# Kernel tuning notes

Measured on AMD Instinct MI355X. Metric: run time of the kernel, lower is better.

The kernel has to match this reference:

```python
import jax, jax.numpy as jnp
import numpy as np

N_HEADS = 16
D_EMBED = 1024


def setup_inputs() -> dict:
    key = jax.random.key(0)
    k_x, k_win, k_bin, k_wout, k_bout = jax.random.split(key, 5)
    B, S, D = 4, 2048, D_EMBED
    # weights stored as (in, out) so y = x @ W + b (equivalent to torch Linear)
    x = jax.random.normal(k_x, (B, S, D), dtype=jnp.float32)
    W_in = jax.random.normal(k_win, (D, 3 * D), dtype=jnp.float32) * (D ** -0.5)
    b_in = jax.random.normal(k_bin, (3 * D,), dtype=jnp.float32) * 0.02
    W_out = jax.random.normal(k_wout, (D, D), dtype=jnp.float32) * (D ** -0.5)
    b_out = jax.random.normal(k_bout, (D,), dtype=jnp.float32) * 0.02
    return {"x": x, "W_in": W_in, "b_in": b_in, "W_out": W_out, "b_out": b_out,
            "causal_mask": 1}


def reference(x, W_in, b_in, W_out, b_out, causal_mask):
    B, S, D = x.shape
    H = N_HEADS
    dh = D // H
    qkv = x @ W_in + b_in                      # [B,S,3D]
    q, k, v = jnp.split(qkv, 3, axis=-1)
    q = q.reshape(B, S, H, dh)
    k = k.reshape(B, S, H, dh)
    v = v.reshape(B, S, H, dh)
    scores = jnp.einsum('bqhd,bkhd->bhqk', q, k)   # [B,H,S,S]
    if causal_mask:
        # original masks with -inf BEFORE scaling; -inf/sqrt(dh) == -inf
        tri = jnp.triu(jnp.ones((S, S), dtype=bool), k=1)
        scores = jnp.where(tri, -jnp.inf, scores)
    scores = scores / jnp.sqrt(jnp.asarray(dh, dtype=scores.dtype))
    attn = jax.nn.softmax(scores, axis=-1)
    out = jnp.einsum('bhqk,bkhd->bqhd', attn, v).reshape(B, S, D)
    return out @ W_out + b_out
```

## Files before the change

kernel.cpp:

```cpp
#include <hip/hip_runtime.h>
#include <hip/hip_bf16.h>
#include <stdint.h>
#include <string.h>

#define S_LEN 2048
#define NH    16
#define DH    64
#define D_EMB 1024
#define CSCALE 0.18033688011112042f

typedef __attribute__((ext_vector_type(8)))  short short8;
typedef __attribute__((ext_vector_type(4)))  float f32x4;
typedef __attribute__((ext_vector_type(16))) float f32x16;
typedef __attribute__((ext_vector_type(4)))  uint32_t u32x4;

__device__ __forceinline__ unsigned short f2bf(float f) {
  uint32_t u = __builtin_bit_cast(uint32_t, f);
  uint32_t r = (u + 0x7FFFu + ((u >> 16) & 1u)) >> 16;
  return (unsigned short)r;
}

__device__ __forceinline__ uint32_t pkbf(float a, float b) {
  float2 f; f.x = a; f.y = b;
  __hip_bfloat162 h = __float22bfloat162_rn(f);
  uint32_t r;
  memcpy(&r, &h, 4);
  return r;
}

__device__ __forceinline__ uint32_t pktr(float a, float b) {
  return __builtin_amdgcn_perm(__builtin_bit_cast(uint32_t, b),
                               __builtin_bit_cast(uint32_t, a), 0x07060302u);
}

__device__ __forceinline__ float fexp2(float x) {
#if __has_builtin(__builtin_amdgcn_exp2f)
  return __builtin_amdgcn_exp2f(x);
#else
  float r;
  asm("v_exp_f32 %0, %1\ns_nop 0" : "=v"(r) : "v"(x));
  return r;
#endif
}

__device__ __forceinline__ void gload16(const void* g, void* l) {
  __builtin_amdgcn_global_load_lds(
      (__attribute__((address_space(1))) void*)(g),
      (__attribute__((address_space(3))) void*)(l),
      16, 0, 0);
}

__device__ __forceinline__ f32x16 mfma32(short8 a, short8 b, f32x16 c) {
  return __builtin_amdgcn_mfma_f32_32x32x16_bf16(a, b, c, 0, 0, 0);
}


__global__ __launch_bounds__(256)
void cvt_bf16(const float* __restrict__ in, unsigned short* __restrict__ out, int n) {
  int i = (blockIdx.x * 256 + threadIdx.x) * 4;
  if (i >= n) return;
  float4 v = *(const float4*)&in[i];
  ushort4 o;
  o.x = f2bf(v.x); o.y = f2bf(v.y); o.z = f2bf(v.z); o.w = f2bf(v.w);
  *(ushort4*)&out[i] = o;
}

__global__ __launch_bounds__(256)
void transpose_cvt(const float* __restrict__ in, unsigned short* __restrict__ out,
                   int R, int C) {
  __shared__ float t[64][65];
  const int nbr = R >> 6;
  const int br = (blockIdx.x % nbr) << 6;
  const int bc = (blockIdx.x / nbr) << 6;
  const int tid = threadIdx.x;
  const int tr = tid >> 4;
  const int tc = (tid & 15) << 2;
#pragma unroll
  for (int i = 0; i < 4; ++i) {
    float4 v = *(const float4*)&in[(size_t)(br + tr + i * 16) * C + bc + tc];
    t[tr + i * 16][tc + 0] = v.x;
    t[tr + i * 16][tc + 1] = v.y;
    t[tr + i * 16][tc + 2] = v.z;
    t[tr + i * 16][tc + 3] = v.w;
  }
  __syncthreads();
#pragma unroll
  for (int i = 0; i < 4; ++i) {
    int c = tr + i * 16;
    ushort4 o;
    o.x = f2bf(t[tc + 0][c]);
    o.y = f2bf(t[tc + 1][c]);
    o.z = f2bf(t[tc + 2][c]);
    o.w = f2bf(t[tc + 3][c]);
    *(ushort4*)&out[(size_t)(bc + c) * R + br + tc] = o;
  }
}


template <int MODE>
__global__ __launch_bounds__(256, 3)
void gemm_bt(const unsigned short* __restrict__ A,
             const unsigned short* __restrict__ Bt,
             const float* __restrict__ bias,
             unsigned short* __restrict__ q_out,
             unsigned short* __restrict__ k_out,
             unsigned short* __restrict__ v_out,
             float* __restrict__ f_out,
             int M, int N, int K) {
  __shared__ __attribute__((aligned(16))) unsigned short As[128 * 64];
  __shared__ __attribute__((aligned(16))) unsigned short Bs[128 * 64];
  const int tid  = threadIdx.x;
  const int lane = tid & 63;
  const int w    = tid >> 6;
  const int grp  = lane >> 4;
  const int lc   = lane & 15;
  const int nbn  = N >> 7;
  const int bm   = blockIdx.x / nbn;
  const int bn   = blockIdx.x % nbn;
  const int wr   = w >> 1, wc = w & 1;

  f32x4 acc[4][4];
#pragma unroll
  for (int m = 0; m < 4; ++m)
#pragma unroll
    for (int n = 0; n < 4; ++n) acc[m][n] = f32x4{0.f, 0.f, 0.f, 0.f};

  const int srow = lane >> 3;
  const int scol = ((lane & 7) ^ srow) * 8;
  const int nkt  = K >> 6;

  for (int kt = 0; kt < nkt; ++kt) {
#pragma unroll
    for (int c = 0; c < 4; ++c) {
      const int rc = w * 32 + c * 8;
      gload16(&A[(size_t)(bm * 128 + rc + srow) * K + kt * 64 + scol],
              (void*)(&As[rc * 64]));
      gload16(&Bt[(size_t)(bn * 128 + rc + srow) * K + kt * 64 + scol],
              (void*)(&Bs[rc * 64]));
    }
    __syncthreads();
#pragma unroll
    for (int kk = 0; kk < 2; ++kk) {
      short8 af[4], bf[4];
#pragma unroll
      for (int m = 0; m < 4; ++m) {
        const int row = wr * 64 + m * 16 + lc;
        const int cb  = ((kk * 4 + grp) ^ (lc & 7)) * 8;
        af[m] = *(const short8*)(&As[row * 64 + cb]);
      }
#pragma unroll
      for (int n = 0; n < 4; ++n) {
        const int row = wc * 64 + n * 16 + lc;
        const int cb  = ((kk * 4 + grp) ^ (lc & 7)) * 8;
        bf[n] = *(const short8*)(&Bs[row * 64 + cb]);
      }
      __builtin_amdgcn_s_setprio(1);
#pragma unroll
      for (int m = 0; m < 4; ++m)
#pragma unroll
        for (int n = 0; n < 4; ++n)
          acc[m][n] = __builtin_amdgcn_mfma_f32_16x16x32_bf16(af[m], bf[n], acc[m][n], 0, 0, 0);
      __builtin_amdgcn_s_setprio(0);
    }
    __syncthreads();
  }

  const int gm0 = bm * 128 + wr * 64;
  const int gn0 = bn * 128 + wc * 64;
  if (MODE == 0) {
    const int seg = gn0 >> 10;
#pragma unroll
    for (int m = 0; m < 4; ++m) {
#pragma unroll
      for (int n = 0; n < 4; ++n) {
        const int gn = gn0 + n * 16 + lc;
        const float bv = bias[gn];
        const int j = gn & 1023;
        const int h = j >> 6, d = j & 63;
        const int gmb = gm0 + m * 16 + grp * 4;
        const int b = gmb >> 11;
        const size_t bhb = ((size_t)(b * NH + h) * 32 + ((gmb & 2047) >> 6)) * 4096;
        if (seg == 2) {
          const size_t vi = bhb + ((d >> 5) * 4 + m) * 512 +
                            ((d & 31) + (grp >> 1) * 32) * 8 + (grp & 1) * 4;
          uint2 dv;
          dv.x = pkbf(acc[m][n][0] + bv, acc[m][n][1] + bv);
          dv.y = pkbf(acc[m][n][2] + bv, acc[m][n][3] + bv);
          *(uint2*)&v_out[vi] = dv;
        } else {
#pragma unroll
          for (int r = 0; r < 4; ++r) {
            const int s = (gmb + r) & 2047;
            float v = acc[m][n][r] + bv;
            if (seg == 0) v *= CSCALE;
            const size_t idx = bhb + (((s >> 5) & 1) * 4 + (d >> 4)) * 512 +
                               ((s & 31) + ((d >> 3) & 1) * 32) * 8 + (d & 7);
            if (seg == 0) q_out[idx] = f2bf(v); else k_out[idx] = f2bf(v);
          }
        }
      }
    }
  } else {
#pragma unroll
    for (int m = 0; m < 4; ++m) {
#pragma unroll
      for (int n = 0; n < 4; ++n) {
        const int gn = gn0 + n * 16 + lc;
        const float bv = bias[gn];
#pragma unroll
        for (int r = 0; r < 4; ++r) {
          const int gm = gm0 + m * 16 + grp * 4 + r;
          f_out[(size_t)gm * N + gn] = acc[m][n][r] + bv;
        }
      }
    }
  }
}


__global__ __launch_bounds__(256, 3)
void attn_fwd9(const unsigned short* __restrict__ Qp,
               const unsigned short* __restrict__ Kp,
               const unsigned short* __restrict__ Vp,
               unsigned short* __restrict__ Aout) {
  __shared__ __attribute__((aligned(16))) unsigned short Ks[2][4096];
  __shared__ __attribute__((aligned(16))) unsigned short Vs[2][4096];
  const int tid  = threadIdx.x;
  const int lane = tid & 63, w = tid >> 6;
  const int q32  = lane & 31;
  const int hi   = lane >> 5;
  const int lof  = lane * 8;
  const int g    = blockIdx.x;
  const int t    = 15 - (g >> 6);
  const int bh   = (((g >> 3) & 7) << 3) | (g & 7);
  const int b    = bh >> 4, h = bh & 15;
  const size_t fb = (size_t)bh * 32;

#define STAGE(bf_, kb_) do {                                          \
    const size_t sb_ = (fb + (size_t)(kb_)) * 4096 + tid * 8;         \
    gload16(Kp + sb_,        (void*)&Ks[bf_][tid * 8]);               \
    gload16(Kp + sb_ + 2048, (void*)&Ks[bf_][2048 + tid * 8]);        \
    gload16(Vp + sb_,        (void*)&Vs[bf_][tid * 8]);               \
    gload16(Vp + sb_ + 2048, (void*)&Vs[bf_][2048 + tid * 8]);        \
  } while (0)

  const int qw0 = t * 128 + w * 32;
  const int qkb = 2 * t + (w >> 1), qsub = w & 1;

  short8 qf[4];
#pragma unroll
  for (int s = 0; s < 4; ++s)
    qf[s] = *(const short8*)(Qp + (fb + qkb) * 4096 + (qsub * 4 + s) * 512 + lof);

  f32x16 oa, ob;
#pragma unroll
  for (int rr = 0; rr < 16; ++rr) { oa[rr] = 0.f; ob[rr] = 0.f; }
  float l = 0.f;

  const int nbt = 2 * t + 2;
  STAGE(0, 0);
  asm volatile("s_waitcnt vmcnt(0)" ::: "memory");
  __syncthreads();
  int buf = 0;

#pragma unroll 1
  for (int kb = 0; kb < nbt; ++kb) {
    if (kb + 1 < nbt) STAGE(buf ^ 1, kb + 1);
    const int kvb = kb << 6;
    if (kvb <= qw0 + 31) {
      const unsigned short* kl = &Ks[buf][0];
      const unsigned short* vl = &Vs[buf][0];

      f32x16 c0, c1;
#pragma unroll
      for (int rr = 0; rr < 16; ++rr) { c0[rr] = 0.f; c1[rr] = -1e30f; }
      const bool do1 = (kvb + 32 <= qw0 + 31);
      __builtin_amdgcn_s_setprio(1);
#pragma unroll
      for (int s = 0; s < 4; ++s) {
        short8 kf = *(const short8*)(kl + s * 512 + lof);
        c0 = mfma32(kf, qf[s], c0);
      }
      if (do1) {
#pragma unroll
        for (int rr = 0; rr < 16; ++rr) c1[rr] = 0.f;
#pragma unroll
        for (int s = 0; s < 4; ++s) {
          short8 kf = *(const short8*)(kl + (4 + s) * 512 + lof);
          c1 = mfma32(kf, qf[s], c1);
        }
      }
      __builtin_amdgcn_s_setprio(0);

      if (kvb + 63 > qw0) {
        const int thr = qw0 + q32 - kvb;
#pragma unroll
        for (int rr = 0; rr < 16; ++rr) {
          const int k0 = (rr & 3) + 8 * (rr >> 2) + 4 * hi;
          if (k0 > thr)      c0[rr] = -1e30f;
          if (k0 + 32 > thr) c1[rr] = -1e30f;
        }
      }

#pragma unroll
      for (int rr = 0; rr < 16; ++rr) c0[rr] = fexp2(c0[rr]);
#pragma unroll
      for (int rr = 0; rr < 16; ++rr) c1[rr] = fexp2(c1[rr]);
      float tp[8];
#pragma unroll
      for (int i = 0; i < 8; ++i)
        tp[i] = (c0[i] + c0[i + 8]) + (c1[i] + c1[i + 8]);
      l += ((tp[0] + tp[1]) + (tp[2] + tp[3])) +
           ((tp[4] + tp[5]) + (tp[6] + tp[7]));

#pragma unroll
      for (int ks = 0; ks < 4; ++ks) {
        if (ks >= 2 && !do1) break;
        uint32_t pA, pB, pC, pD;
        if (ks == 0) {
          pA = pktr(c0[0],  c0[1]);  pB = pktr(c0[2],  c0[3]);
          pC = pktr(c0[4],  c0[5]);  pD = pktr(c0[6],  c0[7]);
        } else if (ks == 1) {
          pA = pktr(c0[8],  c0[9]);  pB = pktr(c0[10], c0[11]);
          pC = pktr(c0[12], c0[13]); pD = pktr(c0[14], c0[15]);
        } else if (ks == 2) {
          pA = pktr(c1[0],  c1[1]);  pB = pktr(c1[2],  c1[3]);
          pC = pktr(c1[4],  c1[5]);  pD = pktr(c1[6],  c1[7]);
        } else {
          pA = pktr(c1[8],  c1[9]);  pB = pktr(c1[10], c1[11]);
          pC = pktr(c1[12], c1[13]); pD = pktr(c1[14], c1[15]);
        }
        auto r0 = __builtin_amdgcn_permlane32_swap(pA, pC, false, false);
        auto r1 = __builtin_amdgcn_permlane32_swap(pB, pD, false, false);
        u32x4 fw; fw[0] = r0[0]; fw[1] = r1[0]; fw[2] = r0[1]; fw[3] = r1[1];
        const short8 frag = __builtin_bit_cast(short8, fw);
        oa = mfma32(*(const short8*)(vl + ks * 512 + lof), frag, oa);
        ob = mfma32(*(const short8*)(vl + (4 + ks) * 512 + lof), frag, ob);
      }
    }
    asm volatile("s_waitcnt vmcnt(0)" ::: "memory");
    __syncthreads();
    buf ^= 1;
  }

  l += __shfl_xor(l, 32);
  const float inv = 1.0f / l;
  unsigned short* ebuf = (unsigned short*)Ks;
  unsigned short* prow = ebuf + (w * 32 + q32) * 64;
  const int swz = (q32 & 7) << 3;
#pragma unroll
  for (int gg = 0; gg < 4; ++gg) {
    const int d0 = 8 * gg + 4 * hi;
    uint2 da, db;
    da.x = pkbf(oa[4 * gg] * inv,     oa[4 * gg + 1] * inv);
    da.y = pkbf(oa[4 * gg + 2] * inv, oa[4 * gg + 3] * inv);
    db.x = pkbf(ob[4 * gg] * inv,     ob[4 * gg + 1] * inv);
    db.y = pkbf(ob[4 * gg + 2] * inv, ob[4 * gg + 3] * inv);
    *(uint2*)&prow[d0 ^ swz]        = da;
    *(uint2*)&prow[(d0 + 32) ^ swz] = db;
  }
  asm volatile("s_waitcnt lgkmcnt(0)" ::: "memory");
  __builtin_amdgcn_sched_barrier(0);
  const int er = lane >> 1, eh = lane & 1;
  const int rswz = (er & 7) << 3;
  const unsigned short* lr = ebuf + (w * 32 + er) * 64;
  unsigned short* op = Aout + ((size_t)(b * S_LEN + qw0 + er)) * D_EMB + h * DH + eh * 32;
#pragma unroll
  for (int jj = 0; jj < 4; ++jj) {
    short8 ov = *(const short8*)&lr[(eh * 32 + jj * 8) ^ rswz];
    *(short8*)(op + jj * 8) = ov;
  }
#undef STAGE
}


extern "C" void kernel_launch(void* const* d_in, const int* in_sizes, int n_in,
                              void* d_out, int out_size, void* d_ws, size_t ws_size,
                              hipStream_t stream) {
  const float* x     = (const float*)d_in[0];
  const float* W_in  = (const float*)d_in[1];
  const float* b_in  = (const float*)d_in[2];
  const float* W_out = (const float*)d_in[3];
  const float* b_out = (const float*)d_in[4];

  char* ws = (char*)d_ws;
  unsigned short* xb  = (unsigned short*)(ws);
  unsigned short* Wti = (unsigned short*)(ws + 16777216);
  unsigned short* Wto = (unsigned short*)(ws + 23068672);
  unsigned short* Qb  = (unsigned short*)(ws + 25165824);
  unsigned short* Kb  = (unsigned short*)(ws + 41943040);
  unsigned short* Vb  = (unsigned short*)(ws + 58720256);
  float* out = (float*)d_out;

  cvt_bf16<<<8192, 256, 0, stream>>>(x, xb, 8388608);
  transpose_cvt<<<16 * 48, 256, 0, stream>>>(W_in, Wti, 1024, 3072);
  transpose_cvt<<<16 * 16, 256, 0, stream>>>(W_out, Wto, 1024, 1024);

  gemm_bt<0><<<64 * 24, 256, 0, stream>>>(xb, Wti, b_in, Qb, Kb, Vb, nullptr,
                                          8192, 3072, 1024);
  attn_fwd9<<<1024, 256, 0, stream>>>(Qb, Kb, Vb, xb);
  gemm_bt<1><<<64 * 8, 256, 0, stream>>>(xb, Wto, b_out, nullptr, nullptr, nullptr, out,
                                         8192, 1024, 1024);
}
```

Before: 152.9 us.

## Triple-buffer K/V tiles in attention and merge prep kernels into one launch

The attention kernel moves from a double-buffered to a triple-buffered K/V LDS pipeline. It prefetches two tiles ahead and waits only on the older loads (vmcnt(4)) instead of draining all outstanding loads each iteration, so global loads overlap more compute. The three preprocessing kernels (x conversion and two weight transposes) are fused into one launch to cut launch overhead. LDS use per block rises from 32 KB to 48 KB, which may reduce the number of resident blocks per CU.

```diff
diff --git a/kernel.cpp b/kernel.cpp
--- a/kernel.cpp
+++ b/kernel.cpp
@@ -56,43 +56,45 @@
 
 
 __global__ __launch_bounds__(256)
-void cvt_bf16(const float* __restrict__ in, unsigned short* __restrict__ out, int n) {
-  int i = (blockIdx.x * 256 + threadIdx.x) * 4;
-  if (i >= n) return;
-  float4 v = *(const float4*)&in[i];
-  ushort4 o;
-  o.x = f2bf(v.x); o.y = f2bf(v.y); o.z = f2bf(v.z); o.w = f2bf(v.w);
-  *(ushort4*)&out[i] = o;
-}
-
-__global__ __launch_bounds__(256)
-void transpose_cvt(const float* __restrict__ in, unsigned short* __restrict__ out,
-                   int R, int C) {
-  __shared__ float t[64][65];
-  const int nbr = R >> 6;
-  const int br = (blockIdx.x % nbr) << 6;
-  const int bc = (blockIdx.x / nbr) << 6;
+void prep(const float* __restrict__ x, unsigned short* __restrict__ xb,
+          const float* __restrict__ W_in, unsigned short* __restrict__ Wti,
+          const float* __restrict__ W_out, unsigned short* __restrict__ Wto) {
+  __shared__ float tsh[64][65];
+  const int blk = blockIdx.x;
   const int tid = threadIdx.x;
+  if (blk < 8192) {
+    const int i = (blk * 256 + tid) * 4;
+    float4 v = *(const float4*)&x[i];
+    ushort4 o;
+    o.x = f2bf(v.x); o.y = f2bf(v.y); o.z = f2bf(v.z); o.w = f2bf(v.w);
+    *(ushort4*)&xb[i] = o;
+    return;
+  }
+  const float* in; unsigned short* out; int C; int bid;
+  if (blk < 8960) { in = W_in;  out = Wti; C = 3072; bid = blk - 8192; }
+  else            { in = W_out; out = Wto; C = 1024; bid = blk - 8960; }
+  const int br = (bid & 15) << 6;
+  const int bc = (bid >> 4) << 6;
   const int tr = tid >> 4;
   const int tc = (tid & 15) << 2;
 #pragma unroll
   for (int i = 0; i < 4; ++i) {
     float4 v = *(const float4*)&in[(size_t)(br + tr + i * 16) * C + bc + tc];
-    t[tr + i * 16][tc + 0] = v.x;
-    t[tr + i * 16][tc + 1] = v.y;
-    t[tr + i * 16][tc + 2] = v.z;
-    t[tr + i * 16][tc + 3] = v.w;
+    tsh[tr + i * 16][tc + 0] = v.x;
+    tsh[tr + i * 16][tc + 1] = v.y;
+    tsh[tr + i * 16][tc + 2] = v.z;
+    tsh[tr + i * 16][tc + 3] = v.w;
   }
   __syncthreads();
 #pragma unroll
   for (int i = 0; i < 4; ++i) {
     int c = tr + i * 16;
     ushort4 o;
-    o.x = f2bf(t[tc + 0][c]);
-    o.y = f2bf(t[tc + 1][c]);
-    o.z = f2bf(t[tc + 2][c]);
-    o.w = f2bf(t[tc + 3][c]);
-    *(ushort4*)&out[(size_t)(bc + c) * R + br + tc] = o;
+    o.x = f2bf(tsh[tc + 0][c]);
+    o.y = f2bf(tsh[tc + 1][c]);
+    o.z = f2bf(tsh[tc + 2][c]);
+    o.w = f2bf(tsh[tc + 3][c]);
+    *(ushort4*)&out[(size_t)(bc + c) * 1024 + br + tc] = o;
   }
 }
 
@@ -219,12 +221,12 @@
 
 
 __global__ __launch_bounds__(256, 3)
-void attn_fwd9(const unsigned short* __restrict__ Qp,
-               const unsigned short* __restrict__ Kp,
-               const unsigned short* __restrict__ Vp,
-               unsigned short* __restrict__ Aout) {
-  __shared__ __attribute__((aligned(16))) unsigned short Ks[2][4096];
-  __shared__ __attribute__((aligned(16))) unsigned short Vs[2][4096];
+void attn_fwd10(const unsigned short* __restrict__ Qp,
+                const unsigned short* __restrict__ Kp,
+                const unsigned short* __restrict__ Vp,
+                unsigned short* __restrict__ Aout) {
+  __shared__ __attribute__((aligned(16))) unsigned short Ks[3][4096];
+  __shared__ __attribute__((aligned(16))) unsigned short Vs[3][4096];
   const int tid  = threadIdx.x;
   const int lane = tid & 63, w = tid >> 6;
   const int q32  = lane & 31;
@@ -259,17 +261,24 @@
 
   const int nbt = 2 * t + 2;
   STAGE(0, 0);
-  asm volatile("s_waitcnt vmcnt(0)" ::: "memory");
-  __syncthreads();
-  int buf = 0;
+  STAGE(1, 1);
+  int cur = 0;
 
 #pragma unroll 1
   for (int kb = 0; kb < nbt; ++kb) {
-    if (kb + 1 < nbt) STAGE(buf ^ 1, kb + 1);
+    if (kb + 1 < nbt) {
+      asm volatile("s_waitcnt vmcnt(4)" ::: "memory");
+    } else {
+      asm volatile("s_waitcnt vmcnt(0)" ::: "memory");
+    }
+    __builtin_amdgcn_sched_barrier(0);
+    __builtin_amdgcn_s_barrier();
+    __builtin_amdgcn_sched_barrier(0);
+
     const int kvb = kb << 6;
     if (kvb <= qw0 + 31) {
-      const unsigned short* kl = &Ks[buf][0];
-      const unsigned short* vl = &Vs[buf][0];
+      const unsigned short* kl = &Ks[cur][0];
+      const unsigned short* vl = &Vs[cur][0];
 
       f32x16 c0, c1;
 #pragma unroll
@@ -338,9 +347,16 @@
         ob = mfma32(*(const short8*)(vl + (4 + ks) * 512 + lof), frag, ob);
       }
     }
-    asm volatile("s_waitcnt vmcnt(0)" ::: "memory");
-    __syncthreads();
-    buf ^= 1;
+
+    asm volatile("s_waitcnt lgkmcnt(0)" ::: "memory");
+    __builtin_amdgcn_sched_barrier(0);
+    __builtin_amdgcn_s_barrier();
+    __builtin_amdgcn_sched_barrier(0);
+    if (kb + 2 < nbt) {
+      const int nx = (cur + 2 >= 3) ? cur - 1 : cur + 2;
+      STAGE(nx, kb + 2);
+    }
+    cur = (cur + 1 == 3) ? 0 : cur + 1;
   }
 
   l += __shfl_xor(l, 32);
@@ -392,13 +408,11 @@
   unsigned short* Vb  = (unsigned short*)(ws + 58720256);
   float* out = (float*)d_out;
 
-  cvt_bf16<<<8192, 256, 0, stream>>>(x, xb, 8388608);
-  transpose_cvt<<<16 * 48, 256, 0, stream>>>(W_in, Wti, 1024, 3072);
-  transpose_cvt<<<16 * 16, 256, 0, stream>>>(W_out, Wto, 1024, 1024);
+  prep<<<9216, 256, 0, stream>>>(x, xb, W_in, Wti, W_out, Wto);
 
   gemm_bt<0><<<64 * 24, 256, 0, stream>>>(xb, Wti, b_in, Qb, Kb, Vb, nullptr,
                                           8192, 3072, 1024);
-  attn_fwd9<<<1024, 256, 0, stream>>>(Qb, Kb, Vb, xb);
+  attn_fwd10<<<1024, 256, 0, stream>>>(Qb, Kb, Vb, xb);
   gemm_bt<1><<<64 * 8, 256, 0, stream>>>(xb, Wto, b_out, nullptr, nullptr, nullptr, out,
                                          8192, 1024, 1024);
 }
```

After: 150.0 us, median of 3. About the same (-1.9%).
